# Optimization experiments

Measured on AMD Instinct MI355X. Metric: run time of the kernel, lower is better.

## Reference

```python
import jax, jax.numpy as jnp
import numpy as np

HIDDEN = 2048
NUM_HEADS = 16
HEAD_DIM = HIDDEN // NUM_HEADS  # 128
B, S = 2, 2048


def setup_inputs() -> dict:
    key = jax.random.key(0)
    ks = jax.random.split(key, 16)
    w = lambda k, shp: (jax.random.normal(k, shp, jnp.float32) * 0.02)
    return {
        "query": jax.random.normal(ks[0], (B, S, HIDDEN), jnp.float32),
        "key": jax.random.normal(ks[1], (B, S, HIDDEN), jnp.float32),
        "value": jax.random.normal(ks[2], (B, S, HIDDEN), jnp.float32),
        "Wq": w(ks[3], (HIDDEN, HIDDEN)), "bq": jnp.zeros((HIDDEN,), jnp.float32),
        "Wk": w(ks[4], (HIDDEN, HIDDEN)), "bk": jnp.zeros((HIDDEN,), jnp.float32),
        "Wv": w(ks[5], (HIDDEN, HIDDEN)), "bv": jnp.zeros((HIDDEN,), jnp.float32),
        "Wo": w(ks[6], (HIDDEN, HIDDEN)), "bo": jnp.zeros((HIDDEN,), jnp.float32),
        "Wf1": w(ks[7], (HEAD_DIM, 2 * HEAD_DIM)), "bf1": jnp.zeros((2 * HEAD_DIM,), jnp.float32),
        "Wf2": w(ks[8], (2 * HEAD_DIM, HEAD_DIM)), "bf2": jnp.zeros((HEAD_DIM,), jnp.float32),
    }


def reference(query, key, value, Wq, bq, Wk, bk, Wv, bv, Wo, bo, Wf1, bf1, Wf2, bf2):
    b, s, _ = query.shape

    def split_heads(x):  # [b,s,H] -> [b,h,s,d]
        return x.reshape(b, s, NUM_HEADS, HEAD_DIM).transpose(0, 2, 1, 3)

    def feature_map(x):  # MLP on last dim: d -> 2d -> relu -> d
        return jax.nn.relu(x @ Wf1 + bf1) @ Wf2 + bf2

    Q = feature_map(split_heads(query @ Wq + bq))
    K = feature_map(split_heads(key @ Wk + bk))
    V = split_heads(value @ Wv + bv)

    # K^T V per head: [b,h,d,e]
    KV = jnp.einsum("bhsd,bhse->bhde", K, V)
    QKV = jnp.einsum("bhsd,bhde->bhse", Q, KV)
    # denominator: sum of all K entries per (b,h) -> scalar per head
    denom = jnp.sum(K, axis=(-2, -1), keepdims=True) + 1e-8
    QKV = QKV / denom

    context = QKV.transpose(0, 2, 1, 3).reshape(b, s, HIDDEN)
    output = context @ Wo + bo

    attn_weights = jnp.full((b, NUM_HEADS, s, s), 1.0 / s, dtype=query.dtype)
    return output, attn_weights
```

## Files before the change

kernel.cpp:

```cpp
#include <hip/hip_runtime.h>


typedef __bf16 bf16_t;
typedef __bf16 bf16x8 __attribute__((ext_vector_type(8)));
typedef __bf16 bf16x4 __attribute__((ext_vector_type(4)));
typedef float  f32x4  __attribute__((ext_vector_type(4)));

#define FILLV (1.0f / 2048.0f)

#define VMCNT3() asm volatile("s_waitcnt vmcnt(3)" ::: "memory")
#define VMCNT2() asm volatile("s_waitcnt vmcnt(2)" ::: "memory")
#define VMCNT0() asm volatile("s_waitcnt vmcnt(0)" ::: "memory")
#define LGKM0()  asm volatile("s_waitcnt lgkmcnt(0)" ::: "memory")
#define BAR()    __builtin_amdgcn_s_barrier()
#define SCHED0() __builtin_amdgcn_sched_barrier(0)

__device__ __forceinline__ void gload16(const void* g, void* l) {
  __builtin_amdgcn_global_load_lds(
      (__attribute__((address_space(1))) void*)(g),
      (__attribute__((address_space(3))) void*)(l), 16, 0, 0);
}

__device__ __forceinline__ void stage_half(const bf16_t* __restrict__ g,
                                           int h, unsigned char* ldsT, int t) {
  const bf16_t* gh = g + (long)h * 128 * 2048;
  unsigned char* lh = ldsT + h * 16384;
#pragma unroll
  for (int i = 0; i < 2; ++i) {
    const int c = t + i * 512;
    const int r = c >> 3;
    const int cc = ((c & 7) ^ (r & 7)) * 8;
    gload16(gh + (long)r * 2048 + cc, lh + c * 16);
  }
}

__device__ __forceinline__ bf16x8 lds_frag(const unsigned char* base,
                                           int row, int kelem) {
  int byte = row * 128 + kelem * 2;
  byte ^= (row & 7) << 4;
  return *(const bf16x8*)(base + byte);
}

__global__ __launch_bounds__(512, 2) void proj_gemm8(
    const bf16_t* __restrict__ A, const bf16_t* __restrict__ Wt,
    const float* __restrict__ bq, const float* __restrict__ bk,
    const float* __restrict__ bv, bf16_t* __restrict__ C,
    float* __restrict__ attn)
{
  __shared__ __align__(16) unsigned char smem[98304];
  const int t = threadIdx.x;
  const int lane = t & 63;
  const int wid = t >> 6;
  const int wr = wid >> 2, wc = wid & 3;
  const int bid = blockIdx.x;
  const int bx = bid & 15, by = bid >> 4;
  const int which = by >> 4;
  const bf16_t* Ab = A + (long)by * 256 * 2048;
  const bf16_t* Bb = Wt + (long)which * 4194304 + (long)bx * 128 * 2048;
  const float* bias = which == 0 ? bq : (which == 1 ? bk : bv);

  const int lr = lane & 15;
  const int l8 = (lane >> 4) * 8;
  const f32x4 fv = {FILLV, FILLV, FILLV, FILLV};

  f32x4 acc[8][2];
#pragma unroll
  for (int i = 0; i < 8; ++i)
#pragma unroll
    for (int j = 0; j < 2; ++j) acc[i][j] = (f32x4){0.f, 0.f, 0.f, 0.f};

  stage_half(Ab, 0, smem, t);
  stage_half(Ab, 1, smem, t);
  stage_half(Bb, 0, smem + 32768, t);

  bf16x8 aF[4][2], bF[2][2];

  for (int kt = 0; kt < 32; ++kt) {
    const int cur = kt & 1;
    unsigned char* curA = smem + cur * 49152;
    unsigned char* curB = curA + 32768;
    unsigned char* nxtA = smem + (cur ^ 1) * 49152;
    unsigned char* nxtB = nxtA + 32768;
    const bool hn = kt < 31;
    const bf16_t* An = Ab + (kt + 1) * 64;
    const bf16_t* Bn = Bb + (kt + 1) * 64;
    const int arow = wr * 128 + lr;
    const int brow = wc * 32 + lr;
    f32x4* fillp = (f32x4*)attn + ((long)kt * 768 + bid) * 1024 + t;

    if (kt == 0)      { stage_half(An, 0, nxtA, t); VMCNT2(); }
    else if (hn)      { stage_half(An, 0, nxtA, t); VMCNT3(); }
    else              { VMCNT0(); }
    BAR();
#pragma unroll
    for (int mi = 0; mi < 4; ++mi)
#pragma unroll
      for (int kk = 0; kk < 2; ++kk)
        aF[mi][kk] = lds_frag(curA, arow + mi * 16, kk * 32 + l8);
#pragma unroll
    for (int kk = 0; kk < 2; ++kk)
      bF[0][kk] = lds_frag(curB, brow, kk * 32 + l8);
    LGKM0(); SCHED0();
    __builtin_amdgcn_s_setprio(1);
#pragma unroll
    for (int mi = 0; mi < 4; ++mi)
#pragma unroll
      for (int kk = 0; kk < 2; ++kk)
        acc[mi][0] = __builtin_amdgcn_mfma_f32_16x16x32_bf16(
            aF[mi][kk], bF[0][kk], acc[mi][0], 0, 0, 0);
    __builtin_amdgcn_s_setprio(0);
    BAR();

    if (hn) stage_half(An, 1, nxtA, t);
    __builtin_nontemporal_store(fv, fillp);
#pragma unroll
    for (int kk = 0; kk < 2; ++kk)
      bF[1][kk] = lds_frag(curB, brow + 16, kk * 32 + l8);
    BAR(); LGKM0(); SCHED0();
    __builtin_amdgcn_s_setprio(1);
#pragma unroll
    for (int mi = 0; mi < 4; ++mi)
#pragma unroll
      for (int kk = 0; kk < 2; ++kk)
        acc[mi][1] = __builtin_amdgcn_mfma_f32_16x16x32_bf16(
            aF[mi][kk], bF[1][kk], acc[mi][1], 0, 0, 0);
    __builtin_amdgcn_s_setprio(0);
    BAR();

    if (hn) stage_half(Bn, 0, nxtB, t);
    __builtin_nontemporal_store(fv, fillp + 512);
#pragma unroll
    for (int mi = 0; mi < 4; ++mi)
#pragma unroll
      for (int kk = 0; kk < 2; ++kk)
        aF[mi][kk] = lds_frag(curA, arow + 64 + mi * 16, kk * 32 + l8);
    BAR(); LGKM0(); SCHED0();
    __builtin_amdgcn_s_setprio(1);
#pragma unroll
    for (int mi = 0; mi < 4; ++mi)
#pragma unroll
      for (int kk = 0; kk < 2; ++kk)
        acc[4 + mi][0] = __builtin_amdgcn_mfma_f32_16x16x32_bf16(
            aF[mi][kk], bF[0][kk], acc[4 + mi][0], 0, 0, 0);
    __builtin_amdgcn_s_setprio(0);
    BAR();

    BAR(); LGKM0(); SCHED0();
    __builtin_amdgcn_s_setprio(1);
#pragma unroll
    for (int mi = 0; mi < 4; ++mi)
#pragma unroll
      for (int kk = 0; kk < 2; ++kk)
        acc[4 + mi][1] = __builtin_amdgcn_mfma_f32_16x16x32_bf16(
            aF[mi][kk], bF[1][kk], acc[4 + mi][1], 0, 0, 0);
    __builtin_amdgcn_s_setprio(0);
    BAR();
  }

  const int row0 = by * 256 + wr * 128;
  const int col0 = bx * 128 + wc * 32;
#pragma unroll
  for (int mi = 0; mi < 8; ++mi) {
#pragma unroll
    for (int ni = 0; ni < 2; ++ni) {
      const int col = col0 + ni * 16 + lr;
      const float bvv = bias[col];
#pragma unroll
      for (int j = 0; j < 4; ++j) {
        const int row = row0 + mi * 16 + (lane >> 4) * 4 + j;
        C[(long)row * 2048 + col] = (bf16_t)(acc[mi][ni][j] + bvv);
      }
    }
  }
}

template<bool RELU, bool OUTF32, bool BIAS, int FILLMODE>
__global__ __launch_bounds__(256) void gemm_bt(
    const bf16_t* __restrict__ A, const bf16_t* __restrict__ Bt,
    const float* __restrict__ bias, void* __restrict__ C,
    int K, int lda, int ldb, int ldc,
    long aBatchB, long aBatchH, long bBatchB, long bBatchH,
    long cBatchB, long cBatchH, int HperB,
    float* __restrict__ attn, long fillBase)
{
  __shared__ bf16_t As[128 * 64];
  __shared__ bf16_t Bs[128 * 64];

  const int z  = blockIdx.z;
  const int zb = z / HperB, zh = z % HperB;
  const bf16_t* Ab = A  + (long)zb * aBatchB + (long)zh * aBatchH
                        + (long)blockIdx.y * 128 * lda;
  const bf16_t* Bb = Bt + (long)zb * bBatchB + (long)zh * bBatchH
                        + (long)blockIdx.x * 128 * ldb;

  const int t = threadIdx.x;
  const int lane = t & 63, w = t >> 6;
  const int wm = (w >> 1) * 64, wn = (w & 1) * 64;
  const int p = ((int)blockIdx.z * gridDim.y + blockIdx.y) * gridDim.x
                + blockIdx.x;

  f32x4 acc[4][4];
#pragma unroll
  for (int i = 0; i < 4; ++i)
#pragma unroll
    for (int j = 0; j < 4; ++j) acc[i][j] = (f32x4){0.f, 0.f, 0.f, 0.f};

  for (int k0 = 0; k0 < K; k0 += 64) {
#pragma unroll
    for (int i = 0; i < 4; ++i) {
      int c = i * 256 + t;
      int row = c >> 3, col = (c & 7) * 8;
      gload16(Ab + (long)row * lda + k0 + col, &As[c * 8]);
      gload16(Bb + (long)row * ldb + k0 + col, &Bs[c * 8]);
    }
    if constexpr (FILLMODE == 1) {
      const f32x4 fv = {FILLV, FILLV, FILLV, FILLV};
      const long nB = (long)gridDim.x * gridDim.y * gridDim.z;
      long s0 = fillBase + (((long)(k0 >> 6) * nB + p) * 2) * 256 + t;
      __builtin_nontemporal_store(fv, (f32x4*)attn + s0);
      __builtin_nontemporal_store(fv, (f32x4*)attn + s0 + 256);
    }
    __syncthreads();
#pragma unroll
    for (int kk = 0; kk < 2; ++kk) {
      bf16x8 af[4], bfr[4];
#pragma unroll
      for (int mi = 0; mi < 4; ++mi)
        af[mi] = *(const bf16x8*)&As[(wm + mi * 16 + (lane & 15)) * 64
                                     + kk * 32 + (lane >> 4) * 8];
#pragma unroll
      for (int ni = 0; ni < 4; ++ni)
        bfr[ni] = *(const bf16x8*)&Bs[(wn + ni * 16 + (lane & 15)) * 64
                                      + kk * 32 + (lane >> 4) * 8];
#pragma unroll
      for (int mi = 0; mi < 4; ++mi)
#pragma unroll
        for (int ni = 0; ni < 4; ++ni)
          acc[mi][ni] = __builtin_amdgcn_mfma_f32_16x16x32_bf16(
              af[mi], bfr[ni], acc[mi][ni], 0, 0, 0);
    }
    __syncthreads();
  }

  const long cb = (long)zb * cBatchB + (long)zh * cBatchH;
  const int row0 = blockIdx.y * 128 + wm;
  const int col0 = blockIdx.x * 128 + wn;
#pragma unroll
  for (int mi = 0; mi < 4; ++mi) {
#pragma unroll
    for (int ni = 0; ni < 4; ++ni) {
      const int col = col0 + ni * 16 + (lane & 15);
      const float bv = BIAS ? bias[col] : 0.f;
#pragma unroll
      for (int j = 0; j < 4; ++j) {
        const int row = row0 + mi * 16 + (lane >> 4) * 4 + j;
        float v = acc[mi][ni][j] + bv;
        if (RELU) v = fmaxf(v, 0.f);
        if (OUTF32) ((float*)C)[cb + (long)row * ldc + col] = v;
        else        ((bf16_t*)C)[cb + (long)row * ldc + col] = (bf16_t)v;
      }
    }
  }
}

__global__ __launch_bounds__(256) void fm_fused(
    const bf16_t* __restrict__ A, const bf16_t* __restrict__ W1t,
    const bf16_t* __restrict__ W2t, const float* __restrict__ b1,
    const float* __restrict__ b2, bf16_t* __restrict__ Out)
{
  __shared__ char Hs[64 * 256 * 2];
  const int t = threadIdx.x, lane = t & 63, w = t >> 6;
  const long r0 = (long)blockIdx.x * 64;
  const int lr = lane & 15, lk = lane >> 4;

  f32x4 acc[4][4];
#pragma unroll
  for (int i = 0; i < 4; ++i)
#pragma unroll
    for (int j = 0; j < 4; ++j) acc[i][j] = (f32x4){0.f, 0.f, 0.f, 0.f};
  const int wn = w * 64;
#pragma unroll
  for (int kk = 0; kk < 4; ++kk) {
    bf16x8 af[4], bfr[4];
#pragma unroll
    for (int mi = 0; mi < 4; ++mi)
      af[mi] = *(const bf16x8*)&A[(r0 + mi * 16 + lr) * 128 + kk * 32 + lk * 8];
#pragma unroll
    for (int ni = 0; ni < 4; ++ni)
      bfr[ni] = *(const bf16x8*)&W1t[(long)(wn + ni * 16 + lr) * 128
                                     + kk * 32 + lk * 8];
#pragma unroll
    for (int mi = 0; mi < 4; ++mi)
#pragma unroll
      for (int ni = 0; ni < 4; ++ni)
        acc[mi][ni] = __builtin_amdgcn_mfma_f32_16x16x32_bf16(
            af[mi], bfr[ni], acc[mi][ni], 0, 0, 0);
  }
#pragma unroll
  for (int ni = 0; ni < 4; ++ni) {
    const int col = wn + ni * 16 + lr;
    const float bvv = b1[col];
#pragma unroll
    for (int mi = 0; mi < 4; ++mi)
#pragma unroll
      for (int j = 0; j < 4; ++j) {
        const int row = mi * 16 + lk * 4 + j;
        float h = fmaxf(acc[mi][ni][j] + bvv, 0.f);
        int byte = (row << 9) + (col << 1);
        byte ^= (row & 7) << 4;
        *(bf16_t*)(Hs + byte) = (bf16_t)h;
      }
  }
  __syncthreads();

  f32x4 acc2[4][2];
#pragma unroll
  for (int i = 0; i < 4; ++i)
#pragma unroll
    for (int j = 0; j < 2; ++j) acc2[i][j] = (f32x4){0.f, 0.f, 0.f, 0.f};
  const int wn2 = w * 32;
#pragma unroll
  for (int kk = 0; kk < 8; ++kk) {
    bf16x8 af[4], bfr[2];
#pragma unroll
    for (int mi = 0; mi < 4; ++mi) {
      const int m = mi * 16 + lr;
      int byte = (m << 9) + kk * 64 + lk * 16;
      byte ^= (m & 7) << 4;
      af[mi] = *(const bf16x8*)(Hs + byte);
    }
#pragma unroll
    for (int ni = 0; ni < 2; ++ni)
      bfr[ni] = *(const bf16x8*)&W2t[(long)(wn2 + ni * 16 + lr) * 256
                                     + kk * 32 + lk * 8];
#pragma unroll
    for (int mi = 0; mi < 4; ++mi)
#pragma unroll
      for (int ni = 0; ni < 2; ++ni)
        acc2[mi][ni] = __builtin_amdgcn_mfma_f32_16x16x32_bf16(
            af[mi], bfr[ni], acc2[mi][ni], 0, 0, 0);
  }
#pragma unroll
  for (int ni = 0; ni < 2; ++ni) {
    const int col = wn2 + ni * 16 + lr;
    const float bvv = b2[col];
#pragma unroll
    for (int mi = 0; mi < 4; ++mi)
#pragma unroll
      for (int j = 0; j < 4; ++j) {
        const int row = mi * 16 + lk * 4 + j;
        Out[(r0 + row) * 128 + col] = (bf16_t)(acc2[mi][ni][j] + bvv);
      }
  }
}

__global__ __launch_bounds__(256) void prep(
    const float* __restrict__ q, const float* __restrict__ k,
    const float* __restrict__ v,
    const float* __restrict__ Wq, const float* __restrict__ Wk,
    const float* __restrict__ Wv, const float* __restrict__ Wo,
    const float* __restrict__ Wf1, const float* __restrict__ Wf2,
    bf16_t* __restrict__ qkv_bf, bf16_t* __restrict__ Wqkv_t,
    bf16_t* __restrict__ Wf1_t, bf16_t* __restrict__ Wf2_t)
{
  const int t = threadIdx.x;
  const int bid = blockIdx.x;
  __shared__ float tile[32][33];

  if (bid < 24576) {
    const float* in = bid < 8192 ? q : (bid < 16384 ? k : v);
    bf16_t* o = qkv_bf + (long)(bid >> 13) * 8388608L;
    long i = ((long)(bid & 8191) * 256 + t) * 4;
    float4 x = *(const float4*)&in[i];
    bf16x4 r = {(bf16_t)x.x, (bf16_t)x.y, (bf16_t)x.z, (bf16_t)x.w};
    *(bf16x4*)&o[i] = r;
    return;
  }

  const int x = t & 31, y = t >> 5;
  const float* W; bf16_t* out; int Kd, Nd, n0, k0;
  if (bid < 40960) {
    const int sub = bid - 24576;
    const int z = sub >> 12, r = sub & 4095;
    W = z == 0 ? Wq : z == 1 ? Wk : z == 2 ? Wv : Wo;
    out = Wqkv_t + (long)z * 4194304L;
    Kd = 2048; Nd = 2048;
    n0 = (r & 63) * 32; k0 = (r >> 6) * 32;
  } else if (bid < 40992) {
    const int sub = bid - 40960;
    W = Wf1; out = Wf1_t; Kd = 128; Nd = 256;
    n0 = (sub & 7) * 32; k0 = (sub >> 3) * 32;
  } else {
    const int sub = bid - 40992;
    W = Wf2; out = Wf2_t; Kd = 256; Nd = 128;
    n0 = (sub & 3) * 32; k0 = (sub >> 2) * 32;
  }
#pragma unroll
  for (int j = 0; j < 32; j += 8)
    tile[y + j][x] = W[(long)(k0 + y + j) * Nd + n0 + x];
  __syncthreads();
#pragma unroll
  for (int j = 0; j < 32; j += 8)
    out[(long)(n0 + y + j) * Kd + k0 + x] = (bf16_t)tile[x][y + j];
}

__global__ __launch_bounds__(256) void kv_partial(
    const bf16_t* __restrict__ Kf, const bf16_t* __restrict__ Vp,
    float* __restrict__ part, float* __restrict__ part_denom) {
  const int z = blockIdx.y, b = z >> 4, h = z & 15;
  const int s0 = blockIdx.x * 256;
  const int t = threadIdx.x;
  __shared__ bf16_t Ks[32 * 128];
  __shared__ bf16_t Vs[32 * 128];
  __shared__ float red[4];
  const bf16_t* Kb = Kf + (long)b * 4194304 + h * 128;
  const bf16_t* Vb = Vp + (long)b * 4194304 + h * 128;
  float acc[8][8];
#pragma unroll
  for (int i = 0; i < 8; ++i)
#pragma unroll
    for (int j = 0; j < 8; ++j) acc[i][j] = 0.f;
  float ksum = 0.f;
  const int d0 = (t & 15) * 8, e0 = (t >> 4) * 8;
  for (int sc = 0; sc < 256; sc += 32) {
#pragma unroll
    for (int i = 0; i < 2; ++i) {
      int idx = (i * 256 + t) * 8;
      int r = idx >> 7, c = idx & 127;
      long g = (long)(s0 + sc + r) * 2048 + c;
      *(bf16x8*)&Ks[r * 128 + c] = *(const bf16x8*)&Kb[g];
      *(bf16x8*)&Vs[r * 128 + c] = *(const bf16x8*)&Vb[g];
    }
    __syncthreads();
    {
      bf16x8 a0 = *(const bf16x8*)&Ks[t * 16];
      bf16x8 a1 = *(const bf16x8*)&Ks[t * 16 + 8];
#pragma unroll
      for (int j = 0; j < 8; ++j) ksum += (float)a0[j] + (float)a1[j];
    }
    for (int s = 0; s < 32; ++s) {
      bf16x8 kv = *(const bf16x8*)&Ks[s * 128 + d0];
      bf16x8 vv = *(const bf16x8*)&Vs[s * 128 + e0];
      float kf[8], vf[8];
#pragma unroll
      for (int i = 0; i < 8; ++i) { kf[i] = (float)kv[i]; vf[i] = (float)vv[i]; }
#pragma unroll
      for (int i = 0; i < 8; ++i)
#pragma unroll
        for (int j = 0; j < 8; ++j) acc[i][j] += vf[i] * kf[j];
    }
    __syncthreads();
  }

#pragma unroll
  for (int off = 32; off; off >>= 1) ksum += __shfl_down(ksum, off, 64);
  if ((t & 63) == 0) red[t >> 6] = ksum;
  __syncthreads();
  if (t == 0)
    part_denom[blockIdx.x * 32 + z] = red[0] + red[1] + red[2] + red[3];

  float* pb = part + ((long)blockIdx.x * 32 + z) * 16384;
#pragma unroll
  for (int i = 0; i < 8; ++i)
#pragma unroll
    for (int j = 0; j < 8; ++j)
      pb[(e0 + i) * 128 + (d0 + j)] = acc[i][j];
}

__global__ __launch_bounds__(256) void kv_reduce(
    const float* __restrict__ part, const float* __restrict__ part_denom,
    bf16_t* __restrict__ KVT) {
  const int z = blockIdx.x >> 4, slice = blockIdx.x & 15;
  const int t = threadIdx.x;
  float dsum = 0.f;
#pragma unroll
  for (int c = 0; c < 8; ++c) dsum += part_denom[c * 32 + z];
  const float inv = 1.0f / (dsum + 1e-8f);
  const long i0 = slice * 1024 + t * 4;
  f32x4 s = {0.f, 0.f, 0.f, 0.f};
#pragma unroll
  for (int c = 0; c < 8; ++c) {
    f32x4 v = *(const f32x4*)&part[((long)c * 32 + z) * 16384 + i0];
    s.x += v.x; s.y += v.y; s.z += v.z; s.w += v.w;
  }
  bf16x4 o = {(bf16_t)(s.x * inv), (bf16_t)(s.y * inv),
              (bf16_t)(s.z * inv), (bf16_t)(s.w * inv)};
  *(bf16x4*)&KVT[(long)z * 16384 + i0] = o;
}

extern "C" void kernel_launch(void* const* d_in, const int* in_sizes, int n_in,
                              void* d_out, int out_size, void* d_ws, size_t ws_size,
                              hipStream_t stream) {
  (void)in_sizes; (void)n_in; (void)out_size; (void)ws_size;
  const float* q   = (const float*)d_in[0];
  const float* k   = (const float*)d_in[1];
  const float* v   = (const float*)d_in[2];
  const float* Wq  = (const float*)d_in[3];
  const float* bq  = (const float*)d_in[4];
  const float* Wk  = (const float*)d_in[5];
  const float* bk  = (const float*)d_in[6];
  const float* Wv  = (const float*)d_in[7];
  const float* bv  = (const float*)d_in[8];
  const float* Wo  = (const float*)d_in[9];
  const float* bo  = (const float*)d_in[10];
  const float* Wf1 = (const float*)d_in[11];
  const float* bf1 = (const float*)d_in[12];
  const float* Wf2 = (const float*)d_in[13];
  const float* bf2 = (const float*)d_in[14];

  bf16_t* P      = (bf16_t*)d_ws;
  bf16_t* qkv_bf = P;
  bf16_t* Wqkv_t = P + 25165824L;
  bf16_t* Wo_t   = P + 37748736L;
  bf16_t* Wf1_t  = P + 41943040L;
  bf16_t* Wf2_t  = P + 41975808L;
  bf16_t* Qp     = P + 42008576L;
  bf16_t* Vp     = P + 58785792L;
  bf16_t* Qf     = P + 83951616L;
  bf16_t* Kf     = P + 92340224L;
  bf16_t* KVT    = P + 100728832L;
  float*  part   = (float*)d_ws;
  float*  part_denom = (float*)d_ws + 4194304L;

  float* out0 = (float*)d_out;
  float* attn = (float*)d_out + 8388608L;

  dim3 blk(256);

  prep<<<41024, blk, 0, stream>>>(q, k, v, Wq, Wk, Wv, Wo, Wf1, Wf2,
                                  qkv_bf, Wqkv_t, Wf1_t, Wf2_t);

  proj_gemm8<<<768, 512, 0, stream>>>(qkv_bf, Wqkv_t, bq, bk, bv, Qp, attn);

  fm_fused<<<2048, blk, 0, stream>>>(Qp, Wf1_t, Wf2_t, bf1, bf2, Qf);

  kv_partial<<<dim3(8, 32), blk, 0, stream>>>(Kf, Vp, part, part_denom);

  kv_reduce<<<512, blk, 0, stream>>>(part, part_denom, KVT);

  gemm_bt<false, false, false, 0><<<dim3(1, 16, 32), blk, 0, stream>>>(
      Qf, KVT, nullptr, Vp, 128, 2048, 128, 2048,
      4194304L, 128L, 262144L, 16384L, 4194304L, 128L, 16,
      nullptr, 0);

  gemm_bt<false, true, true, 1><<<dim3(16, 32, 1), blk, 0, stream>>>(
      Vp, Wo_t, bo, out0, 2048, 2048, 2048, 2048, 0, 0, 0, 0, 0, 0, 1,
      attn, 25165824L);
}
```

Before: 350.6 us.

## Route output projection through the pipelined 256x128 gemm8 kernel

Templates the QKV projection kernel so it can also serve the output projection, with fp32 output, a single bias and a fill offset. The simple 128x128 gemm_bt path, and its attn-fill stores, are replaced by this double-buffered, swizzled-LDS kernel launched on 256 blocks. It also tightens the async-load wait counts from vmcnt(3) to vmcnt(2) and drops one lgkmcnt wait. The aim is better data reuse and load/compute overlap in the large Wo GEMM. The trade-offs are fewer, larger blocks and possible ordering hazards from the relaxed waits.

```diff
diff --git a/kernel.cpp b/kernel.cpp
--- a/kernel.cpp
+++ b/kernel.cpp
@@ -8,7 +8,6 @@
 
 #define FILLV (1.0f / 2048.0f)
 
-#define VMCNT3() asm volatile("s_waitcnt vmcnt(3)" ::: "memory")
 #define VMCNT2() asm volatile("s_waitcnt vmcnt(2)" ::: "memory")
 #define VMCNT0() asm volatile("s_waitcnt vmcnt(0)" ::: "memory")
 #define LGKM0()  asm volatile("s_waitcnt lgkmcnt(0)" ::: "memory")
@@ -41,11 +40,12 @@
   return *(const bf16x8*)(base + byte);
 }
 
-__global__ __launch_bounds__(512, 2) void proj_gemm8(
+template<bool OUTF32, bool TRIPLE>
+__global__ __launch_bounds__(512, 2) void gemm8(
     const bf16_t* __restrict__ A, const bf16_t* __restrict__ Wt,
-    const float* __restrict__ bq, const float* __restrict__ bk,
-    const float* __restrict__ bv, bf16_t* __restrict__ C,
-    float* __restrict__ attn)
+    const float* __restrict__ b0, const float* __restrict__ b1,
+    const float* __restrict__ b2, void* __restrict__ C,
+    float* __restrict__ attn, long fillBase)
 {
   __shared__ __align__(16) unsigned char smem[98304];
   const int t = threadIdx.x;
@@ -54,14 +54,15 @@
   const int wr = wid >> 2, wc = wid & 3;
   const int bid = blockIdx.x;
   const int bx = bid & 15, by = bid >> 4;
-  const int which = by >> 4;
+  const int which = TRIPLE ? (by >> 4) : 0;
   const bf16_t* Ab = A + (long)by * 256 * 2048;
   const bf16_t* Bb = Wt + (long)which * 4194304 + (long)bx * 128 * 2048;
-  const float* bias = which == 0 ? bq : (which == 1 ? bk : bv);
+  const float* bias = TRIPLE ? (which == 0 ? b0 : (which == 1 ? b1 : b2)) : b0;
 
   const int lr = lane & 15;
   const int l8 = (lane >> 4) * 8;
   const f32x4 fv = {FILLV, FILLV, FILLV, FILLV};
+  const int nblk = gridDim.x;
 
   f32x4 acc[8][2];
 #pragma unroll
@@ -86,11 +87,10 @@
     const bf16_t* Bn = Bb + (kt + 1) * 64;
     const int arow = wr * 128 + lr;
     const int brow = wc * 32 + lr;
-    f32x4* fillp = (f32x4*)attn + ((long)kt * 768 + bid) * 1024 + t;
-
-    if (kt == 0)      { stage_half(An, 0, nxtA, t); VMCNT2(); }
-    else if (hn)      { stage_half(An, 0, nxtA, t); VMCNT3(); }
-    else              { VMCNT0(); }
+    f32x4* fillp = (f32x4*)attn + fillBase + ((long)kt * nblk + bid) * 1024 + t;
+
+    if (hn) { stage_half(An, 0, nxtA, t); VMCNT2(); }
+    else    { VMCNT0(); }
     BAR();
 #pragma unroll
     for (int mi = 0; mi < 4; ++mi)
@@ -145,7 +145,7 @@
     __builtin_amdgcn_s_setprio(0);
     BAR();
 
-    BAR(); LGKM0(); SCHED0();
+    BAR(); SCHED0();
     __builtin_amdgcn_s_setprio(1);
 #pragma unroll
     for (int mi = 0; mi < 4; ++mi)
@@ -168,20 +168,19 @@
 #pragma unroll
       for (int j = 0; j < 4; ++j) {
         const int row = row0 + mi * 16 + (lane >> 4) * 4 + j;
-        C[(long)row * 2048 + col] = (bf16_t)(acc[mi][ni][j] + bvv);
+        const float v = acc[mi][ni][j] + bvv;
+        if (OUTF32) ((float*)C)[(long)row * 2048 + col] = v;
+        else        ((bf16_t*)C)[(long)row * 2048 + col] = (bf16_t)v;
       }
     }
   }
 }
 
-template<bool RELU, bool OUTF32, bool BIAS, int FILLMODE>
 __global__ __launch_bounds__(256) void gemm_bt(
     const bf16_t* __restrict__ A, const bf16_t* __restrict__ Bt,
-    const float* __restrict__ bias, void* __restrict__ C,
-    int K, int lda, int ldb, int ldc,
+    bf16_t* __restrict__ C, int K, int lda, int ldb, int ldc,
     long aBatchB, long aBatchH, long bBatchB, long bBatchH,
-    long cBatchB, long cBatchH, int HperB,
-    float* __restrict__ attn, long fillBase)
+    long cBatchB, long cBatchH, int HperB)
 {
   __shared__ bf16_t As[128 * 64];
   __shared__ bf16_t Bs[128 * 64];
@@ -196,8 +195,6 @@
   const int t = threadIdx.x;
   const int lane = t & 63, w = t >> 6;
   const int wm = (w >> 1) * 64, wn = (w & 1) * 64;
-  const int p = ((int)blockIdx.z * gridDim.y + blockIdx.y) * gridDim.x
-                + blockIdx.x;
 
   f32x4 acc[4][4];
 #pragma unroll
@@ -213,13 +210,6 @@
       gload16(Ab + (long)row * lda + k0 + col, &As[c * 8]);
       gload16(Bb + (long)row * ldb + k0 + col, &Bs[c * 8]);
     }
-    if constexpr (FILLMODE == 1) {
-      const f32x4 fv = {FILLV, FILLV, FILLV, FILLV};
-      const long nB = (long)gridDim.x * gridDim.y * gridDim.z;
-      long s0 = fillBase + (((long)(k0 >> 6) * nB + p) * 2) * 256 + t;
-      __builtin_nontemporal_store(fv, (f32x4*)attn + s0);
-      __builtin_nontemporal_store(fv, (f32x4*)attn + s0 + 256);
-    }
     __syncthreads();
 #pragma unroll
     for (int kk = 0; kk < 2; ++kk) {
@@ -250,14 +240,10 @@
 #pragma unroll
     for (int ni = 0; ni < 4; ++ni) {
       const int col = col0 + ni * 16 + (lane & 15);
-      const float bv = BIAS ? bias[col] : 0.f;
 #pragma unroll
       for (int j = 0; j < 4; ++j) {
         const int row = row0 + mi * 16 + (lane >> 4) * 4 + j;
-        float v = acc[mi][ni][j] + bv;
-        if (RELU) v = fmaxf(v, 0.f);
-        if (OUTF32) ((float*)C)[cb + (long)row * ldc + col] = v;
-        else        ((bf16_t*)C)[cb + (long)row * ldc + col] = (bf16_t)v;
+        C[cb + (long)row * ldc + col] = (bf16_t)acc[mi][ni][j];
       }
     }
   }
@@ -530,7 +516,8 @@
   prep<<<41024, blk, 0, stream>>>(q, k, v, Wq, Wk, Wv, Wo, Wf1, Wf2,
                                   qkv_bf, Wqkv_t, Wf1_t, Wf2_t);
 
-  proj_gemm8<<<768, 512, 0, stream>>>(qkv_bf, Wqkv_t, bq, bk, bv, Qp, attn);
+  gemm8<false, true><<<768, 512, 0, stream>>>(
+      qkv_bf, Wqkv_t, bq, bk, bv, Qp, attn, 0L);
 
   fm_fused<<<2048, blk, 0, stream>>>(Qp, Wf1_t, Wf2_t, bf1, bf2, Qf);
 
@@ -538,12 +525,10 @@
 
   kv_reduce<<<512, blk, 0, stream>>>(part, part_denom, KVT);
 
-  gemm_bt<false, false, false, 0><<<dim3(1, 16, 32), blk, 0, stream>>>(
-      Qf, KVT, nullptr, Vp, 128, 2048, 128, 2048,
-      4194304L, 128L, 262144L, 16384L, 4194304L, 128L, 16,
-      nullptr, 0);
-
-  gemm_bt<false, true, true, 1><<<dim3(16, 32, 1), blk, 0, stream>>>(
-      Vp, Wo_t, bo, out0, 2048, 2048, 2048, 2048, 0, 0, 0, 0, 0, 0, 1,
-      attn, 25165824L);
-}
+  gemm_bt<<<dim3(1, 16, 32), blk, 0, stream>>>(
+      Qf, KVT, Vp, 128, 2048, 128, 2048,
+      4194304L, 128L, 262144L, 16384L, 4194304L, 128L, 16);
+
+  gemm8<true, false><<<256, 512, 0, stream>>>(
+      Vp, Wo_t, bo, nullptr, nullptr, out0, attn, 25165824L);
+}
```

After: 343.0 us. 2.2% less time.
